# Kernel tuning notes

Hardware: AMD Instinct MI355X
Metric: run time of the kernel (lower is better)

The kernel has to match this reference:

```python
import jax, jax.numpy as jnp
import numpy as np

NUM_HEADS = 12

def setup_inputs() -> dict:
    key = jax.random.key(0)
    ks = jax.random.split(key, 6)
    B, N, C = 4, 2048, 768
    s = 0.02
    return {
        "x": jax.random.normal(ks[0], (B, N, C), jnp.float32),
        "y": jax.random.normal(ks[1], (B, N, C), jnp.float32),
        "Wq": jax.random.normal(ks[2], (C, C), jnp.float32) * s,
        "Wkv": jax.random.normal(ks[3], (2 * C, C), jnp.float32) * s,
        "tau_param": jnp.asarray(1.0, jnp.float32),
        "Wproj": jax.random.normal(ks[4], (C, C), jnp.float32) * s,
        "bproj": jnp.zeros((C,), jnp.float32),
    }

def reference(x, y, Wq, Wkv, tau_param, Wproj, bproj):
    B, N, C = x.shape
    H = NUM_HEADS
    D = C // H
    scale = D ** -0.5
    # q: [B,H,N,D]
    q = (x @ Wq.T).reshape(B, N, H, D).transpose(0, 2, 1, 3) * scale
    kv = (y @ Wkv.T).reshape(B, N, 2, H, D).transpose(2, 0, 3, 1, 4)
    k, v = kv[0], kv[1]
    tau = jax.nn.softplus(tau_param) + 1e-6
    attn = jnp.einsum("bhnd,bhmd->bhnm", q, k) / tau  # [B,H,N,N]
    attn = jax.nn.softmax(attn, axis=-1)
    out = jnp.einsum("bhnm,bhmd->bhnd", attn, v)  # [B,H,N,D]
    out = out.transpose(0, 2, 1, 3).reshape(B, N, C)
    return out @ Wproj.T + bproj
```

## Files before the change

kernel.cpp:

```cpp
#include <hip/hip_runtime.h>
#include <math.h>

typedef unsigned short u16;
typedef unsigned int u32;
typedef __fp16 fp16x2 __attribute__((ext_vector_type(2)));
typedef _Float16 half8 __attribute__((ext_vector_type(8)));
typedef float f32x4 __attribute__((ext_vector_type(4)));

#define NH   12
#define SEQ  2048
#define CDIM 768

__device__ __forceinline__ u16 f2h(float f) {
  _Float16 h = (_Float16)f;
  return __builtin_bit_cast(u16, h);
}
__device__ __forceinline__ u32 pk2(float a, float b) {
  fp16x2 h = __builtin_amdgcn_cvt_pkrtz(a, b);
  return __builtin_bit_cast(u32, h);
}
__device__ __forceinline__ void dma16(const u16* g, u16* l) {
  __builtin_amdgcn_global_load_lds(
      (const __attribute__((address_space(1))) u32*)g,
      (__attribute__((address_space(3))) u32*)l, 16, 0, 0);
}

__global__ __launch_bounds__(256) void cvt_f32_f16(const float* __restrict__ in,
                                                   u16* __restrict__ out, int n) {
  int i = (blockIdx.x * 256 + threadIdx.x) * 4;
  if (i < n) {
    float4 f = *(const float4*)(in + i);
    *(uint2*)(out + i) = make_uint2(pk2(f.x, f.y), pk2(f.z, f.w));
  }
}
__global__ __launch_bounds__(256) void cvt_f32_f16_scale(const float* __restrict__ in,
                                                         u16* __restrict__ out,
                                                         const float* __restrict__ taup, int n) {
  float t = *taup;
  float sp = (t > 20.f) ? t : log1pf(expf(t));
  float s = (0.125f / (sp + 1e-6f)) * 1.44269504088896340736f;
  int i = (blockIdx.x * 256 + threadIdx.x) * 4;
  if (i < n) {
    float4 f = *(const float4*)(in + i);
    *(uint2*)(out + i) = make_uint2(pk2(f.x * s, f.y * s), pk2(f.z * s, f.w * s));
  }
}

template<int MODE>
__global__ __launch_bounds__(256, 2) void gemm_nt(
    const u16* __restrict__ A, const u16* __restrict__ B,
    u16* __restrict__ out0, u16* __restrict__ out1,
    float* __restrict__ outf, const float* __restrict__ bias,
    int M, int N, int K)
{
  __shared__ __align__(16) u16 As[2][128 * 64];
  __shared__ __align__(16) u16 Bs[2][128 * 64];
  const int tid = threadIdx.x;
  const int wave = tid >> 6, lane = tid & 63;
  const int quad = lane >> 4, l16 = lane & 15;
  const int wr = wave >> 1, wc = wave & 1;
  const int row0 = blockIdx.x * 128, col0 = blockIdx.y * 128;

  const int sub = lane >> 3;
  const int csw = ((lane & 7) ^ sub) * 8;

  f32x4 acc[4][4] = {};

  auto stage = [&](int k0, int bsel) {
    u16* Asp = As[bsel];
    u16* Bsp = Bs[bsel];
    #pragma unroll
    for (int i = 0; i < 4; i++) {
      int ii = wave * 4 + i;
      dma16(A + (size_t)(row0 + ii * 8 + sub) * K + k0 + csw, Asp + ii * 512);
      dma16(B + (size_t)(col0 + ii * 8 + sub) * K + k0 + csw, Bsp + ii * 512);
    }
  };

  stage(0, 0);
  __syncthreads();

  const int nk = K >> 6;
  for (int t = 0; t < nk; t++) {
    const int cur = t & 1;
    if (t + 1 < nk) stage((t + 1) << 6, cur ^ 1);
    const u16* Asp = As[cur];
    const u16* Bsp = Bs[cur];
    #pragma unroll
    for (int ks = 0; ks < 2; ks++) {
      half8 af[4], bfr[4];
      #pragma unroll
      for (int mt = 0; mt < 4; mt++)
        af[mt] = *(const half8*)&Asp[(wr * 64 + mt * 16 + l16) * 64 + (((ks * 4 + quad) ^ (l16 & 7)) * 8)];
      #pragma unroll
      for (int nt = 0; nt < 4; nt++)
        bfr[nt] = *(const half8*)&Bsp[(wc * 64 + nt * 16 + l16) * 64 + (((ks * 4 + quad) ^ (l16 & 7)) * 8)];
      #pragma unroll
      for (int mt = 0; mt < 4; mt++)
        #pragma unroll
        for (int nt = 0; nt < 4; nt++)
          acc[mt][nt] = __builtin_amdgcn_mfma_f32_16x16x32_f16(af[mt], bfr[nt], acc[mt][nt], 0, 0, 0);
    }
    __syncthreads();
  }

  #pragma unroll
  for (int mt = 0; mt < 4; mt++)
  #pragma unroll
  for (int nt = 0; nt < 4; nt++)
  #pragma unroll
  for (int r = 0; r < 4; r++) {
    int gm = row0 + wr * 64 + mt * 16 + quad * 4 + r;
    int gn = col0 + wc * 64 + nt * 16 + l16;
    float v = acc[mt][nt][r];
    if (MODE == 0) {
      int b = gm >> 11, n = gm & 2047;
      int h = gn >> 6, d = gn & 63;
      out0[(((size_t)(b * NH + h)) * SEQ + n) * 64 + d] = f2h(v);
    } else if (MODE == 1) {
      int b = gm >> 11, n = gm & 2047;
      if (gn < CDIM) {
        int h = gn >> 6, d = gn & 63;
        out0[(((size_t)(b * NH + h)) * SEQ + n) * 64 + d] = f2h(v);
      } else {
        int c = gn - CDIM;
        int h = c >> 6, d = c & 63;
        out1[(((size_t)(b * NH + h)) * 64 + d) * SEQ + n] = f2h(v);
      }
    } else {
      outf[(size_t)gm * N + gn] = v + bias[gn];
    }
  }
}

__global__ __launch_bounds__(256, 3) void attn_kernel(
    const u16* __restrict__ Q, const u16* __restrict__ Kb,
    const u16* __restrict__ Vtg, u16* __restrict__ Ob)
{
  constexpr int LDP = 72;
  __shared__ __align__(16) u16 Ks[2][64 * 64];
  __shared__ __align__(16) u16 Vs[2][64 * 64];
  __shared__ __align__(16) u16 Ps[4 * 16 * LDP];

  const int bid = (blockIdx.x & 7) * 96 + (blockIdx.x >> 3);
  const int qt = bid & 15;
  const int bh = bid >> 4;
  const int b = bh / NH, h = bh % NH;
  const u16* Qp = Q   + (size_t)bh * SEQ * 64;
  const u16* Kp = Kb  + (size_t)bh * SEQ * 64;
  const u16* Vp = Vtg + (size_t)bh * 64 * SEQ;

  const int tid = threadIdx.x;
  const int wave = tid >> 6, lane = tid & 63;
  const int quad = lane >> 4, l16 = lane & 15;
  const int sub = lane >> 3;
  const int csw = ((lane & 7) ^ sub) * 8;
  u16* Pw = Ps + wave * 16 * LDP;

  half8 vone;
  #pragma unroll
  for (int j = 0; j < 8; j++) vone[j] = (_Float16)1.0f;

  half8 qf[2][2];
  #pragma unroll
  for (int mt = 0; mt < 2; mt++)
    #pragma unroll
    for (int ks = 0; ks < 2; ks++)
      qf[mt][ks] = *(const half8*)(Qp + (size_t)(qt * 128 + wave * 32 + mt * 16 + l16) * 64 + ks * 32 + quad * 8);

  f32x4 oacc[2][4] = {};
  f32x4 lacc[2] = {};

  auto stage = [&](int kt, int bsel) {
    #pragma unroll
    for (int i = 0; i < 2; i++) {
      int ii = wave * 2 + i;
      dma16(Kp + (size_t)(kt * 64 + ii * 8 + sub) * 64 + csw, &Ks[bsel][ii * 512]);
      dma16(Vp + (size_t)(ii * 8 + sub) * SEQ + kt * 64 + csw, &Vs[bsel][ii * 512]);
    }
  };

  stage(0, 0);
  __syncthreads();

  for (int kt = 0; kt < SEQ / 64; kt++) {
    const int cur = kt & 1;
    if (kt + 1 < SEQ / 64) stage(kt + 1, cur ^ 1);
    const u16* Ksp = Ks[cur];
    const u16* Vsp = Vs[cur];

    f32x4 sacc[2][4] = {};
    __builtin_amdgcn_s_setprio(1);
    #pragma unroll
    for (int ks = 0; ks < 2; ks++) {
      #pragma unroll
      for (int ntk = 0; ntk < 4; ntk++) {
        half8 kf = *(const half8*)&Ksp[(ntk * 16 + l16) * 64 + (((ks * 4 + quad) ^ (l16 & 7)) * 8)];
        #pragma unroll
        for (int mt = 0; mt < 2; mt++)
          sacc[mt][ntk] = __builtin_amdgcn_mfma_f32_16x16x32_f16(kf, qf[mt][ks], sacc[mt][ntk], 0, 0, 0);
      }
    }
    __builtin_amdgcn_s_setprio(0);

    half8 pf[2][2];
    #pragma unroll
    for (int mt = 0; mt < 2; mt++) {
      #pragma unroll
      for (int ntk = 0; ntk < 4; ntk++) {
        float p0 = __builtin_amdgcn_exp2f(sacc[mt][ntk][0]);
        float p1 = __builtin_amdgcn_exp2f(sacc[mt][ntk][1]);
        float p2 = __builtin_amdgcn_exp2f(sacc[mt][ntk][2]);
        float p3 = __builtin_amdgcn_exp2f(sacc[mt][ntk][3]);
        *(uint2*)(&Pw[l16 * LDP + ntk * 16 + quad * 4]) = make_uint2(pk2(p0, p1), pk2(p2, p3));
      }
      pf[mt][0] = *(const half8*)&Pw[l16 * LDP + quad * 8];
      pf[mt][1] = *(const half8*)&Pw[l16 * LDP + 32 + quad * 8];
    }

    __builtin_amdgcn_s_setprio(1);
    #pragma unroll
    for (int ks = 0; ks < 2; ks++) {
      #pragma unroll
      for (int dt = 0; dt < 4; dt++) {
        half8 vf = *(const half8*)&Vsp[(dt * 16 + l16) * 64 + (((ks * 4 + quad) ^ (l16 & 7)) * 8)];
        #pragma unroll
        for (int mt = 0; mt < 2; mt++)
          oacc[mt][dt] = __builtin_amdgcn_mfma_f32_16x16x32_f16(pf[mt][ks], vf, oacc[mt][dt], 0, 0, 0);
      }
      #pragma unroll
      for (int mt = 0; mt < 2; mt++)
        lacc[mt] = __builtin_amdgcn_mfma_f32_16x16x32_f16(pf[mt][ks], vone, lacc[mt], 0, 0, 0);
    }
    __builtin_amdgcn_s_setprio(0);

    __syncthreads();
  }

  #pragma unroll
  for (int mt = 0; mt < 2; mt++) {
    #pragma unroll
    for (int r = 0; r < 4; r++) {
      float inv = 1.0f / lacc[mt][r];
      int n = qt * 128 + wave * 32 + mt * 16 + quad * 4 + r;
      size_t base = ((size_t)b * SEQ + n) * CDIM + h * 64;
      #pragma unroll
      for (int dt = 0; dt < 4; dt++)
        Ob[base + dt * 16 + l16] = f2h(oacc[mt][dt][r] * inv);
    }
  }
}

extern "C" void kernel_launch(void* const* d_in, const int* in_sizes, int n_in,
                              void* d_out, int out_size, void* d_ws, size_t ws_size,
                              hipStream_t stream)
{
  const float* x     = (const float*)d_in[0];
  const float* y     = (const float*)d_in[1];
  const float* Wq    = (const float*)d_in[2];
  const float* Wkv   = (const float*)d_in[3];
  const float* taup  = (const float*)d_in[4];
  const float* Wproj = (const float*)d_in[5];
  const float* bproj = (const float*)d_in[6];
  float* out = (float*)d_out;

  char* ws = (char*)d_ws;
  size_t off = 0;
  auto alloc = [&](size_t bytes) { char* p = ws + off; off += bytes; return p; };
  u16* xh  = (u16*)alloc(8192ull * 768 * 2);
  u16* yh  = (u16*)alloc(8192ull * 768 * 2);
  u16* wqh = (u16*)alloc(768ull * 768 * 2);
  u16* wkh = (u16*)alloc(1536ull * 768 * 2);
  u16* wph = (u16*)alloc(768ull * 768 * 2);
  u16* qb  = (u16*)alloc(8192ull * 768 * 2);
  u16* kb  = (u16*)alloc(8192ull * 768 * 2);
  u16* vtb = (u16*)alloc(8192ull * 768 * 2);
  u16* ao  = (u16*)alloc(8192ull * 768 * 2);

  cvt_f32_f16<<<6144, 256, 0, stream>>>(x, xh, 8192 * 768);
  cvt_f32_f16<<<6144, 256, 0, stream>>>(y, yh, 8192 * 768);
  cvt_f32_f16_scale<<<576, 256, 0, stream>>>(Wq, wqh, taup, 768 * 768);
  cvt_f32_f16<<<1152, 256, 0, stream>>>(Wkv, wkh, 1536 * 768);
  cvt_f32_f16<<<576, 256, 0, stream>>>(Wproj, wph, 768 * 768);

  gemm_nt<0><<<dim3(64, 6), 256, 0, stream>>>(xh, wqh, qb, nullptr, nullptr, nullptr, 8192, 768, 768);
  gemm_nt<1><<<dim3(64, 12), 256, 0, stream>>>(yh, wkh, kb, vtb, nullptr, nullptr, 8192, 1536, 768);
  attn_kernel<<<dim3(48 * 16), 256, 0, stream>>>(qb, kb, vtb, ao);
  gemm_nt<2><<<dim3(64, 6), 256, 0, stream>>>(ao, wph, nullptr, nullptr, out, bproj, 8192, 768, 768);
}
```

Measured before the change: 250.9 us.

## Fuse conversion launches, merge Q/KV GEMMs, shrink tiles for more blocks

Collapses the five fp32-to-fp16 conversion launches into two, and merges the Q and KV projection GEMMs into one launch. GEMM tiles shrink to 128x64 with three blocks per CU, and the V-transpose epilogue now writes packed 8-byte stores. The attention kernel now gives each wave 16 query rows instead of 32, doubling the grid to 1536 blocks at four blocks per CU. The P scratch moves to a swizzled unpadded layout to avoid LDS bank conflicts. Together these aim to cut launch overhead and raise occupancy, at the cost of less register-level reuse per block in both GEMM and attention.

```diff
diff --git a/kernel.cpp b/kernel.cpp
--- a/kernel.cpp
+++ b/kernel.cpp
@@ -25,80 +25,105 @@
       (__attribute__((address_space(3))) u32*)l, 16, 0, 0);
 }
 
-__global__ __launch_bounds__(256) void cvt_f32_f16(const float* __restrict__ in,
-                                                   u16* __restrict__ out, int n) {
-  int i = (blockIdx.x * 256 + threadIdx.x) * 4;
-  if (i < n) {
-    float4 f = *(const float4*)(in + i);
-    *(uint2*)(out + i) = make_uint2(pk2(f.x, f.y), pk2(f.z, f.w));
-  }
-}
-__global__ __launch_bounds__(256) void cvt_f32_f16_scale(const float* __restrict__ in,
-                                                         u16* __restrict__ out,
-                                                         const float* __restrict__ taup, int n) {
-  float t = *taup;
-  float sp = (t > 20.f) ? t : log1pf(expf(t));
-  float s = (0.125f / (sp + 1e-6f)) * 1.44269504088896340736f;
-  int i = (blockIdx.x * 256 + threadIdx.x) * 4;
-  if (i < n) {
-    float4 f = *(const float4*)(in + i);
-    *(uint2*)(out + i) = make_uint2(pk2(f.x * s, f.y * s), pk2(f.z * s, f.w * s));
-  }
+__global__ __launch_bounds__(256) void cvt_xy(const float* __restrict__ x,
+                                              const float* __restrict__ y,
+                                              u16* __restrict__ xh, u16* __restrict__ yh) {
+  const long NEL = 8192l * 768;
+  long i = ((long)blockIdx.x * 256 + threadIdx.x) * 4;
+  const float* in = (i < NEL) ? x : y;
+  u16* out = (i < NEL) ? xh : yh;
+  long j = (i < NEL) ? i : i - NEL;
+  float4 f = *(const float4*)(in + j);
+  *(uint2*)(out + j) = make_uint2(pk2(f.x, f.y), pk2(f.z, f.w));
+}
+__global__ __launch_bounds__(256) void cvt_w(const float* __restrict__ Wq,
+                                             const float* __restrict__ Wkv,
+                                             const float* __restrict__ Wp,
+                                             const float* __restrict__ taup,
+                                             u16* __restrict__ wqh, u16* __restrict__ wkh,
+                                             u16* __restrict__ wph) {
+  const long E1 = 768l * 768, E2 = E1 + 1536l * 768;
+  long i = ((long)blockIdx.x * 256 + threadIdx.x) * 4;
+  const float* in; u16* out; long j; float s;
+  if (i < E1) {
+    float t = *taup;
+    float sp = (t > 20.f) ? t : log1pf(expf(t));
+    s = (0.125f / (sp + 1e-6f)) * 1.44269504088896340736f;
+    in = Wq; out = wqh; j = i;
+  } else if (i < E2) {
+    s = 1.f; in = Wkv; out = wkh; j = i - E1;
+  } else {
+    s = 1.f; in = Wp; out = wph; j = i - E2;
+  }
+  float4 f = *(const float4*)(in + j);
+  *(uint2*)(out + j) = make_uint2(pk2(f.x * s, f.y * s), pk2(f.z * s, f.w * s));
 }
 
 template<int MODE>
-__global__ __launch_bounds__(256, 2) void gemm_nt(
-    const u16* __restrict__ A, const u16* __restrict__ B,
-    u16* __restrict__ out0, u16* __restrict__ out1,
-    float* __restrict__ outf, const float* __restrict__ bias,
-    int M, int N, int K)
+__global__ __launch_bounds__(256, 3) void gemm_k(
+    const u16* __restrict__ A0, const u16* __restrict__ A1,
+    const u16* __restrict__ B0, const u16* __restrict__ B1,
+    u16* __restrict__ oq, u16* __restrict__ ok, u16* __restrict__ ovt,
+    float* __restrict__ outf, const float* __restrict__ bias)
 {
   __shared__ __align__(16) u16 As[2][128 * 64];
-  __shared__ __align__(16) u16 Bs[2][128 * 64];
+  __shared__ __align__(16) u16 Bs[2][64 * 64];
   const int tid = threadIdx.x;
   const int wave = tid >> 6, lane = tid & 63;
   const int quad = lane >> 4, l16 = lane & 15;
   const int wr = wave >> 1, wc = wave & 1;
-  const int row0 = blockIdx.x * 128, col0 = blockIdx.y * 128;
+  const int row0 = blockIdx.x * 128;
+  const int by = blockIdx.y;
+
+  const u16* A; const u16* Bm; int cb;
+  if (MODE == 0) {
+    if (by < 12) { A = A0; Bm = B0; cb = by; }
+    else         { A = A1; Bm = B1; cb = by - 12; }
+  } else {
+    A = A0; Bm = B0; cb = by;
+  }
+  const int col0 = cb * 64;
 
   const int sub = lane >> 3;
   const int csw = ((lane & 7) ^ sub) * 8;
 
-  f32x4 acc[4][4] = {};
+  f32x4 acc[4][2] = {};
 
   auto stage = [&](int k0, int bsel) {
-    u16* Asp = As[bsel];
-    u16* Bsp = Bs[bsel];
     #pragma unroll
     for (int i = 0; i < 4; i++) {
       int ii = wave * 4 + i;
-      dma16(A + (size_t)(row0 + ii * 8 + sub) * K + k0 + csw, Asp + ii * 512);
-      dma16(B + (size_t)(col0 + ii * 8 + sub) * K + k0 + csw, Bsp + ii * 512);
+      dma16(A + (size_t)(row0 + ii * 8 + sub) * 768 + k0 + csw, &As[bsel][ii * 512]);
+    }
+    #pragma unroll
+    for (int i = 0; i < 2; i++) {
+      int ii = wave * 2 + i;
+      dma16(Bm + (size_t)(col0 + ii * 8 + sub) * 768 + k0 + csw, &Bs[bsel][ii * 512]);
     }
   };
 
   stage(0, 0);
   __syncthreads();
 
-  const int nk = K >> 6;
-  for (int t = 0; t < nk; t++) {
+  #pragma unroll 1
+  for (int t = 0; t < 12; t++) {
     const int cur = t & 1;
-    if (t + 1 < nk) stage((t + 1) << 6, cur ^ 1);
+    if (t + 1 < 12) stage((t + 1) << 6, cur ^ 1);
     const u16* Asp = As[cur];
     const u16* Bsp = Bs[cur];
     #pragma unroll
     for (int ks = 0; ks < 2; ks++) {
-      half8 af[4], bfr[4];
+      half8 af[4], bfr[2];
       #pragma unroll
       for (int mt = 0; mt < 4; mt++)
         af[mt] = *(const half8*)&Asp[(wr * 64 + mt * 16 + l16) * 64 + (((ks * 4 + quad) ^ (l16 & 7)) * 8)];
       #pragma unroll
-      for (int nt = 0; nt < 4; nt++)
-        bfr[nt] = *(const half8*)&Bsp[(wc * 64 + nt * 16 + l16) * 64 + (((ks * 4 + quad) ^ (l16 & 7)) * 8)];
+      for (int nt = 0; nt < 2; nt++)
+        bfr[nt] = *(const half8*)&Bsp[(wc * 32 + nt * 16 + l16) * 64 + (((ks * 4 + quad) ^ (l16 & 7)) * 8)];
       #pragma unroll
       for (int mt = 0; mt < 4; mt++)
         #pragma unroll
-        for (int nt = 0; nt < 4; nt++)
+        for (int nt = 0; nt < 2; nt++)
           acc[mt][nt] = __builtin_amdgcn_mfma_f32_16x16x32_f16(af[mt], bfr[nt], acc[mt][nt], 0, 0, 0);
     }
     __syncthreads();
@@ -107,44 +132,48 @@
   #pragma unroll
   for (int mt = 0; mt < 4; mt++)
   #pragma unroll
-  for (int nt = 0; nt < 4; nt++)
-  #pragma unroll
-  for (int r = 0; r < 4; r++) {
-    int gm = row0 + wr * 64 + mt * 16 + quad * 4 + r;
-    int gn = col0 + wc * 64 + nt * 16 + l16;
-    float v = acc[mt][nt][r];
+  for (int nt = 0; nt < 2; nt++) {
+    int gm0 = row0 + wr * 64 + mt * 16 + quad * 4;
+    int gn = col0 + wc * 32 + nt * 16 + l16;
+    f32x4 v = acc[mt][nt];
     if (MODE == 0) {
-      int b = gm >> 11, n = gm & 2047;
-      int h = gn >> 6, d = gn & 63;
-      out0[(((size_t)(b * NH + h)) * SEQ + n) * 64 + d] = f2h(v);
-    } else if (MODE == 1) {
-      int b = gm >> 11, n = gm & 2047;
-      if (gn < CDIM) {
+      int b = gm0 >> 11, n0 = gm0 & 2047;
+      if (by < 12) {
         int h = gn >> 6, d = gn & 63;
-        out0[(((size_t)(b * NH + h)) * SEQ + n) * 64 + d] = f2h(v);
+        size_t base = (((size_t)(b * NH + h)) * SEQ + n0) * 64 + d;
+        #pragma unroll
+        for (int r = 0; r < 4; r++) oq[base + (size_t)r * 64] = f2h(v[r]);
+      } else if (gn < CDIM) {
+        int h = gn >> 6, d = gn & 63;
+        size_t base = (((size_t)(b * NH + h)) * SEQ + n0) * 64 + d;
+        #pragma unroll
+        for (int r = 0; r < 4; r++) ok[base + (size_t)r * 64] = f2h(v[r]);
       } else {
         int c = gn - CDIM;
         int h = c >> 6, d = c & 63;
-        out1[(((size_t)(b * NH + h)) * 64 + d) * SEQ + n] = f2h(v);
+        *(uint2*)&ovt[(((size_t)(b * NH + h)) * 64 + d) * SEQ + n0] =
+            make_uint2(pk2(v[0], v[1]), pk2(v[2], v[3]));
       }
     } else {
-      outf[(size_t)gm * N + gn] = v + bias[gn];
-    }
-  }
-}
-
-__global__ __launch_bounds__(256, 3) void attn_kernel(
+      float bv = bias[gn];
+      #pragma unroll
+      for (int r = 0; r < 4; r++)
+        outf[(size_t)(gm0 + r) * CDIM + gn] = v[r] + bv;
+    }
+  }
+}
+
+__global__ __launch_bounds__(256, 4) void attn_kernel(
     const u16* __restrict__ Q, const u16* __restrict__ Kb,
     const u16* __restrict__ Vtg, u16* __restrict__ Ob)
 {
-  constexpr int LDP = 72;
   __shared__ __align__(16) u16 Ks[2][64 * 64];
   __shared__ __align__(16) u16 Vs[2][64 * 64];
-  __shared__ __align__(16) u16 Ps[4 * 16 * LDP];
-
-  const int bid = (blockIdx.x & 7) * 96 + (blockIdx.x >> 3);
-  const int qt = bid & 15;
-  const int bh = bid >> 4;
+  __shared__ __align__(16) u16 Ps[4 * 16 * 64];
+
+  const int bid = (blockIdx.x & 7) * 192 + (blockIdx.x >> 3);
+  const int qt = bid & 31;
+  const int bh = bid >> 5;
   const int b = bh / NH, h = bh % NH;
   const u16* Qp = Q   + (size_t)bh * SEQ * 64;
   const u16* Kp = Kb  + (size_t)bh * SEQ * 64;
@@ -155,21 +184,19 @@
   const int quad = lane >> 4, l16 = lane & 15;
   const int sub = lane >> 3;
   const int csw = ((lane & 7) ^ sub) * 8;
-  u16* Pw = Ps + wave * 16 * LDP;
+  u16* Pw = Ps + wave * 16 * 64;
 
   half8 vone;
   #pragma unroll
   for (int j = 0; j < 8; j++) vone[j] = (_Float16)1.0f;
 
-  half8 qf[2][2];
-  #pragma unroll
-  for (int mt = 0; mt < 2; mt++)
-    #pragma unroll
-    for (int ks = 0; ks < 2; ks++)
-      qf[mt][ks] = *(const half8*)(Qp + (size_t)(qt * 128 + wave * 32 + mt * 16 + l16) * 64 + ks * 32 + quad * 8);
-
-  f32x4 oacc[2][4] = {};
-  f32x4 lacc[2] = {};
+  half8 qf[2];
+  #pragma unroll
+  for (int ks = 0; ks < 2; ks++)
+    qf[ks] = *(const half8*)(Qp + (size_t)(qt * 64 + wave * 16 + l16) * 64 + ks * 32 + quad * 8);
+
+  f32x4 oacc[4] = {};
+  f32x4 lacc = {};
 
   auto stage = [&](int kt, int bsel) {
     #pragma unroll
@@ -189,34 +216,31 @@
     const u16* Ksp = Ks[cur];
     const u16* Vsp = Vs[cur];
 
-    f32x4 sacc[2][4] = {};
+    f32x4 sacc[4] = {};
     __builtin_amdgcn_s_setprio(1);
     #pragma unroll
     for (int ks = 0; ks < 2; ks++) {
       #pragma unroll
       for (int ntk = 0; ntk < 4; ntk++) {
         half8 kf = *(const half8*)&Ksp[(ntk * 16 + l16) * 64 + (((ks * 4 + quad) ^ (l16 & 7)) * 8)];
-        #pragma unroll
-        for (int mt = 0; mt < 2; mt++)
-          sacc[mt][ntk] = __builtin_amdgcn_mfma_f32_16x16x32_f16(kf, qf[mt][ks], sacc[mt][ntk], 0, 0, 0);
+        sacc[ntk] = __builtin_amdgcn_mfma_f32_16x16x32_f16(kf, qf[ks], sacc[ntk], 0, 0, 0);
       }
     }
     __builtin_amdgcn_s_setprio(0);
 
-    half8 pf[2][2];
-    #pragma unroll
-    for (int mt = 0; mt < 2; mt++) {
-      #pragma unroll
-      for (int ntk = 0; ntk < 4; ntk++) {
-        float p0 = __builtin_amdgcn_exp2f(sacc[mt][ntk][0]);
-        float p1 = __builtin_amdgcn_exp2f(sacc[mt][ntk][1]);
-        float p2 = __builtin_amdgcn_exp2f(sacc[mt][ntk][2]);
-        float p3 = __builtin_amdgcn_exp2f(sacc[mt][ntk][3]);
-        *(uint2*)(&Pw[l16 * LDP + ntk * 16 + quad * 4]) = make_uint2(pk2(p0, p1), pk2(p2, p3));
-      }
-      pf[mt][0] = *(const half8*)&Pw[l16 * LDP + quad * 8];
-      pf[mt][1] = *(const half8*)&Pw[l16 * LDP + 32 + quad * 8];
-    }
+    #pragma unroll
+    for (int ntk = 0; ntk < 4; ntk++) {
+      float p0 = __builtin_amdgcn_exp2f(sacc[ntk][0]);
+      float p1 = __builtin_amdgcn_exp2f(sacc[ntk][1]);
+      float p2 = __builtin_amdgcn_exp2f(sacc[ntk][2]);
+      float p3 = __builtin_amdgcn_exp2f(sacc[ntk][3]);
+      *(uint2*)&Pw[l16 * 64 + (((ntk * 2 + (quad >> 1)) ^ (l16 & 7)) * 8) + (quad & 1) * 4] =
+          make_uint2(pk2(p0, p1), pk2(p2, p3));
+    }
+    half8 pf[2];
+    #pragma unroll
+    for (int ks = 0; ks < 2; ks++)
+      pf[ks] = *(const half8*)&Pw[l16 * 64 + (((ks * 4 + quad) ^ (l16 & 7)) * 8)];
 
     __builtin_amdgcn_s_setprio(1);
     #pragma unroll
@@ -224,13 +248,9 @@
       #pragma unroll
       for (int dt = 0; dt < 4; dt++) {
         half8 vf = *(const half8*)&Vsp[(dt * 16 + l16) * 64 + (((ks * 4 + quad) ^ (l16 & 7)) * 8)];
-        #pragma unroll
-        for (int mt = 0; mt < 2; mt++)
-          oacc[mt][dt] = __builtin_amdgcn_mfma_f32_16x16x32_f16(pf[mt][ks], vf, oacc[mt][dt], 0, 0, 0);
+        oacc[dt] = __builtin_amdgcn_mfma_f32_16x16x32_f16(pf[ks], vf, oacc[dt], 0, 0, 0);
       }
-      #pragma unroll
-      for (int mt = 0; mt < 2; mt++)
-        lacc[mt] = __builtin_amdgcn_mfma_f32_16x16x32_f16(pf[mt][ks], vone, lacc[mt], 0, 0, 0);
+      lacc = __builtin_amdgcn_mfma_f32_16x16x32_f16(pf[ks], vone, lacc, 0, 0, 0);
     }
     __builtin_amdgcn_s_setprio(0);
 
@@ -238,16 +258,13 @@
   }
 
   #pragma unroll
-  for (int mt = 0; mt < 2; mt++) {
-    #pragma unroll
-    for (int r = 0; r < 4; r++) {
-      float inv = 1.0f / lacc[mt][r];
-      int n = qt * 128 + wave * 32 + mt * 16 + quad * 4 + r;
-      size_t base = ((size_t)b * SEQ + n) * CDIM + h * 64;
-      #pragma unroll
-      for (int dt = 0; dt < 4; dt++)
-        Ob[base + dt * 16 + l16] = f2h(oacc[mt][dt][r] * inv);
-    }
+  for (int r = 0; r < 4; r++) {
+    float inv = 1.0f / lacc[r];
+    int n = qt * 64 + wave * 16 + quad * 4 + r;
+    size_t base = ((size_t)b * SEQ + n) * CDIM + h * 64;
+    #pragma unroll
+    for (int dt = 0; dt < 4; dt++)
+      Ob[base + dt * 16 + l16] = f2h(oacc[dt][r] * inv);
   }
 }
 
@@ -277,14 +294,10 @@
   u16* vtb = (u16*)alloc(8192ull * 768 * 2);
   u16* ao  = (u16*)alloc(8192ull * 768 * 2);
 
-  cvt_f32_f16<<<6144, 256, 0, stream>>>(x, xh, 8192 * 768);
-  cvt_f32_f16<<<6144, 256, 0, stream>>>(y, yh, 8192 * 768);
-  cvt_f32_f16_scale<<<576, 256, 0, stream>>>(Wq, wqh, taup, 768 * 768);
-  cvt_f32_f16<<<1152, 256, 0, stream>>>(Wkv, wkh, 1536 * 768);
-  cvt_f32_f16<<<576, 256, 0, stream>>>(Wproj, wph, 768 * 768);
-
-  gemm_nt<0><<<dim3(64, 6), 256, 0, stream>>>(xh, wqh, qb, nullptr, nullptr, nullptr, 8192, 768, 768);
-  gemm_nt<1><<<dim3(64, 12), 256, 0, stream>>>(yh, wkh, kb, vtb, nullptr, nullptr, 8192, 1536, 768);
-  attn_kernel<<<dim3(48 * 16), 256, 0, stream>>>(qb, kb, vtb, ao);
-  gemm_nt<2><<<dim3(64, 6), 256, 0, stream>>>(ao, wph, nullptr, nullptr, out, bproj, 8192, 768, 768);
-}
+  cvt_xy<<<12288, 256, 0, stream>>>(x, y, xh, yh);
+  cvt_w<<<2304, 256, 0, stream>>>(Wq, Wkv, Wproj, taup, wqh, wkh, wph);
+
+  gemm_k<0><<<dim3(64, 36), 256, 0, stream>>>(xh, yh, wqh, wkh, qb, kb, vtb, nullptr, nullptr);
+  attn_kernel<<<dim3(1536), 256, 0, stream>>>(qb, kb, vtb, ao);
+  gemm_k<2><<<dim3(64, 12), 256, 0, stream>>>(ao, nullptr, wph, nullptr, nullptr, nullptr, nullptr, out, bproj);
+}
```

Result: faster. 238.1 us (-5.1%).
